# Optimization experiments

Hardware: AMD Instinct MI355X
Metric: run time of the kernel (lower is better)

## Reference

```python
import jax, jax.numpy as jnp
import numpy as np

SIZE = 256
R = 896          # total radial bins = nodes per sample (128 + 4*64 + 16*32)
LMAX = 510       # widest folded ring row (i=127 -> 4i+2)
WMAX = LMAX - 1  # conv output width (kernel=2)
HID = 32         # ConvAutoEncoder hidden channels (create_layers default)
ENC = 10         # hidden_encoder (per-bin embedding dim)
GCN_H = 64
NCLS = 10
B = 8
EPS = 7168       # edges per sample (avg degree 8)
PAD = 3 * SIZE * SIZE  # padding gather index -> zero column


def _reshape_2d(arr, border):
    # verbatim port of reshape_2d, applied to index arrays
    ptr_st, ptr_end = border, len(arr) - border
    d1 = list(arr[:ptr_st]); d2 = list(arr[ptr_end:])
    itt = 4
    while ptr_st != ptr_end:
        (d1 if itt > 2 else d2).append(arr[ptr_st])
        ptr_st += 1; itt -= 1
        if itt == 0:
            itt = 4
    return np.stack([d1, d2])


def build_static():
    # For each radial bin rad in 0..895: flat gather indices (into the
    # concatenated 3*256*256 per-sample maps) in boolean-mask (row-major)
    # order, folded by reshape_2d to (2, 4i+2), padded to LMAX with PAD.
    idx = np.full((R, 2, LMAX), PAD, np.int32)
    band = np.zeros(R, np.int32)
    rad = 0
    for m, coef in enumerate([1, 2, 4]):
        step = SIZE // coef
        c = step / 2 - 0.5
        ii, jj = np.meshgrid(np.arange(step), np.arange(step), indexing='ij')
        d = (np.maximum(np.abs(ii - c), np.abs(jj - c)) // 1).astype(int)  # create_circular
        for by in range(coef):
            for bx in range(coef):
                flat = m * SIZE * SIZE + (by * step + ii) * SIZE + (bx * step + jj)
                for i in range(step // 2):
                    sel = flat[d == i]                    # row-major ring pixels (8i+4)
                    two = _reshape_2d(sel, 2 + 2 * i)     # (2, 4i+2)
                    L = two.shape[1]
                    idx[rad, :, :L] = two
                    band[rad] = L - 1                     # band_length = 4i+1
                    rad += 1
    return idx, band


def gcn_conv(x, W, b, src, dst, ew, n):
    # torch_geometric GCNConv: add self loops (w=1), symmetric norm, aggregate at dst
    loop = jnp.arange(n)
    s = jnp.concatenate([src, loop])
    t = jnp.concatenate([dst, loop])
    w = jnp.concatenate([ew, jnp.ones((n,), x.dtype)])
    deg = jax.ops.segment_sum(w, t, num_segments=n)
    dinv = jnp.where(deg > 0, jax.lax.rsqrt(jnp.maximum(deg, 1e-12)), 0.0)
    norm = dinv[s] * w * dinv[t]
    xw = x @ W
    return jax.ops.segment_sum(norm[:, None] * xw[s], t, num_segments=n) + b


def setup_inputs() -> dict:
    key = jax.random.key(0)
    ks = jax.random.split(key, 12)
    idx_np, band = build_static()
    x = jax.random.normal(ks[0], (B, 3, SIZE, SIZE), jnp.float32)
    base = jax.random.randint(ks[1], (2, B, EPS), 0, R)
    edge_index = (base + (jnp.arange(B) * R)[None, :, None]).reshape(2, -1)
    batch_vec = jnp.arange(B * R, dtype=jnp.int32) // R
    Wconv = jax.random.normal(ks[2], (R, HID, 2, 2), jnp.float32) * 0.3
    bconv = jax.random.normal(ks[3], (R, HID), jnp.float32) * 0.05
    # decoder padded to WMAX, zeroed beyond each bin's band length (exact math)
    mask = (np.arange(WMAX)[None, :] < band[:, None]).astype(np.float32)
    Wdec = jax.random.normal(ks[4], (R, ENC, HID, WMAX), jnp.float32) * 0.02
    Wdec = Wdec * jnp.asarray(mask)[:, None, None, :]
    bdec = jax.random.normal(ks[5], (R, ENC), jnp.float32) * 0.05
    edge_w = jax.random.normal(ks[6], (EPS,), jnp.float32)
    Wg1 = jax.random.normal(ks[7], (ENC, GCN_H), jnp.float32) * (1.0 / np.sqrt(ENC))
    bg1 = jnp.zeros((GCN_H,), jnp.float32)
    Wg2 = jax.random.normal(ks[8], (GCN_H, GCN_H), jnp.float32) * (1.0 / np.sqrt(GCN_H))
    bg2 = jnp.zeros((GCN_H,), jnp.float32)
    Wl = jax.random.normal(ks[9], (GCN_H, NCLS), jnp.float32) * (1.0 / np.sqrt(GCN_H))
    bl = jnp.zeros((NCLS,), jnp.float32)
    return dict(x=x, edge_index=edge_index, batch_vec=batch_vec, idx=jnp.asarray(idx_np),
                Wconv=Wconv, bconv=bconv, Wdec=Wdec, bdec=bdec, edge_w=edge_w,
                Wg1=Wg1, bg1=bg1, Wg2=Wg2, bg2=bg2, Wl=Wl, bl=bl)


def reference(x, edge_index, batch_vec, idx, Wconv, bconv, Wdec, bdec, edge_w,
              Wg1, bg1, Wg2, bg2, Wl, bl):
    b = x.shape[0]
    n = b * R
    # --- get_embedding: batched radial-bin gather + per-bin 2x2 conv + linear ---
    xp = jnp.concatenate([x.reshape(b, -1), jnp.zeros((b, 1), x.dtype)], axis=1)
    vals = xp[:, idx]                                         # (B,R,2,LMAX)
    win = jnp.stack([vals[..., :-1], vals[..., 1:]], axis=-1)  # (B,R,2,WMAX,2) = b r kh w kw
    h = jax.nn.relu(jnp.einsum('brhwk,rchk->brcw', win, Wconv) + bconv[:, :, None])
    emb = jnp.einsum('brcw,rocw->bro', h, Wdec) + bdec         # (B,R,ENC)
    nodes = emb.reshape(n, ENC)
    # --- GCN: trainable sigmoid edge weights tiled per sample ---
    ew = jax.nn.sigmoid(jnp.tile(edge_w, b))
    src, dst = edge_index[0], edge_index[1]
    h1 = jax.nn.relu(gcn_conv(nodes, Wg1, bg1, src, dst, ew, n))
    h2 = gcn_conv(h1, Wg2, bg2, src, dst, ew, n)
    pooled = jax.ops.segment_sum(h2, batch_vec, num_segments=b) / R  # global_mean_pool (equal sizes)
    # dropout p=0.1 in eval mode -> identity
    return jax.nn.softmax(pooled @ Wl + bl, axis=1)
```

## Files before the change

kernel.cpp:

```cpp
#include <hip/hip_runtime.h>

static constexpr int kR    = 896;
static constexpr int kLMAX = 510;
static constexpr int kWMAX = 509;
static constexpr int kHID  = 32;
static constexpr int kENC  = 10;
static constexpr int kGH   = 64;
static constexpr int kNCLS = 10;
static constexpr int kB    = 8;
static constexpr int kEPS  = 7168;
static constexpr int kN    = kB * kR;
static constexpr int kE    = kB * kEPS;
static constexpr int kPAD  = 3 * 256 * 256;

constexpr int band_of(int r) {
    int i = (r < 128) ? r : (r < 384) ? ((r - 128) & 63) : ((r - 384) & 31);
    return 4 * i + 1;
}
__device__ __forceinline__ int band_dev(int r) {
    int i = (r < 128) ? r : (r < 384) ? ((r - 128) & 63) : ((r - 384) & 31);
    return 4 * i + 1;
}

static constexpr int kCHUNK = 128;
constexpr int count_chunks() {
    int n = 0;
    for (int r = 0; r < kR; ++r) n += (band_of(r) + kCHUNK - 1) / kCHUNK;
    return n;
}
static constexpr int kNCHUNK = count_chunks();
static_assert(kNCHUNK == 1216, "chunk count");

struct CE { short r; short w0; };
struct Tab { CE e[kNCHUNK]; };
constexpr Tab make_tab() {
    Tab t{};
    int n = 0;
    for (int r = 0; r < kR; ++r)
        for (int w0 = 0; w0 < band_of(r); w0 += kCHUNK) {
            t.e[n].r = (short)r; t.e[n].w0 = (short)w0; ++n;
        }
    return t;
}
__device__ __constant__ Tab g_tab = make_tab();

static constexpr size_t OFF_EMB  = 0;
static constexpr size_t OFF_DEG  = OFF_EMB + 71680;
static constexpr size_t OFF_CNT  = OFF_DEG + 7168;
static constexpr size_t OFF_POOL = OFF_CNT + 7168;
static constexpr size_t kMEMSET_FLOATS = OFF_POOL + 512;
static constexpr size_t OFF_DINV = kMEMSET_FLOATS;
static constexpr size_t OFF_CSUM = OFF_DINV + 7168;
static constexpr size_t OFF_OFFS = OFF_CSUM + 7168;
static constexpr size_t OFF_WOFF = OFF_OFFS + 7169;
static constexpr size_t OFF_CSRC = OFF_WOFF + 7169;
static constexpr size_t OFF_CNRM = OFF_CSRC + 57344;
static constexpr size_t OFF_XW1  = OFF_CNRM + 57344;
static constexpr size_t OFF_XT   = (OFF_XW1 + 458752 + 7) & ~(size_t)7;

__device__ __forceinline__ float sigmoidf_(float v) { return 1.0f / (1.0f + expf(-v)); }

__global__ __launch_bounds__(256)
void k_xpose(const float* __restrict__ x, const int* __restrict__ ei,
             const float* __restrict__ edge_w,
             float* __restrict__ xt, float* __restrict__ deg, int* __restrict__ cnt)
{
    const int bid = blockIdx.x;
    const int tid = threadIdx.x;
    if (bid < kPAD / 256) {
        const int j = bid * 256 + tid;
        float4 lo, hi;
        lo.x = x[(size_t)0 * kPAD + j]; lo.y = x[(size_t)1 * kPAD + j];
        lo.z = x[(size_t)2 * kPAD + j]; lo.w = x[(size_t)3 * kPAD + j];
        hi.x = x[(size_t)4 * kPAD + j]; hi.y = x[(size_t)5 * kPAD + j];
        hi.z = x[(size_t)6 * kPAD + j]; hi.w = x[(size_t)7 * kPAD + j];
        float4* dst = (float4*)&xt[(size_t)j * 8];
        dst[0] = lo; dst[1] = hi;
    } else {
        const int e = (bid - kPAD / 256) * 256 + tid;
        if (e < kE) {
            const int t = ei[kE + e];
            atomicAdd(&deg[t], sigmoidf_(edge_w[e % kEPS]));
            atomicAdd(&cnt[t], 1);
        }
    }
}

__global__ __launch_bounds__(320, 4)
void k_conv_emb(const float* __restrict__ xt, const int* __restrict__ idx,
                const float* __restrict__ Wconv, const float* __restrict__ bconv,
                const float* __restrict__ Wdec, float* __restrict__ emb)
{
    const int bid = blockIdx.x;
    const int tid = threadIdx.x;

    const int r     = g_tab.e[bid].r;
    const int w0    = g_tab.e[bid].w0;
    const int bandr = band_dev(r);
    const int wc    = min(kCHUNK, bandr - w0);

    __shared__ float vals[2][kB][kCHUNK + 1];
    __shared__ float wconv_s[kHID * 4];
    __shared__ float bconv_s[kHID];

    if (tid < 128) wconv_s[tid] = Wconv[r * 128 + tid];
    else if (tid < 160) bconv_s[tid - 128] = bconv[r * kHID + (tid - 128)];

    if (tid < 2 * (kCHUNK + 1)) {
        const int hh = tid >= (kCHUNK + 1);
        const int li = tid - hh * (kCHUNK + 1);
        const int j = (li <= wc) ? idx[(r * 2 + hh) * kLMAX + w0 + li] : kPAD;
        float4 lo = {0, 0, 0, 0}, hi = {0, 0, 0, 0};
        if ((unsigned)j < (unsigned)kPAD) {
            const float4* src = (const float4*)&xt[(size_t)j * 8];
            lo = src[0]; hi = src[1];
        }
        vals[hh][0][li] = lo.x; vals[hh][1][li] = lo.y;
        vals[hh][2][li] = lo.z; vals[hh][3][li] = lo.w;
        vals[hh][4][li] = hi.x; vals[hh][5][li] = hi.y;
        vals[hh][6][li] = hi.z; vals[hh][7][li] = hi.w;
    }
    __syncthreads();

    const int wave = tid >> 6, lane = tid & 63;
    const int o0 = wave * 2;
    const float* Wd0 = Wdec + ((size_t)(r * kENC + o0) * kHID) * kWMAX;
    const float* Wd1 = Wd0 + (size_t)kHID * kWMAX;

    float acc0[8] = {0,0,0,0,0,0,0,0}, acc1[8] = {0,0,0,0,0,0,0,0};

    #pragma unroll
    for (int st = 0; st < 2; ++st) {
        const int wl = st * 64 + lane;
        if (st * 64 >= wc) break;
        const bool valid = (wl < wc);
        const int w = w0 + wl;

        float v00[8], v01[8], v10[8], v11[8];
        #pragma unroll
        for (int b = 0; b < 8; ++b) {
            v00[b] = vals[0][b][wl]; v01[b] = vals[0][b][wl + 1];
            v10[b] = vals[1][b][wl]; v11[b] = vals[1][b][wl + 1];
        }

        #pragma unroll 8
        for (int c = 0; c < kHID; ++c) {
            const float wd0 = valid ? Wd0[(size_t)c * kWMAX + w] : 0.0f;
            const float wd1 = valid ? Wd1[(size_t)c * kWMAX + w] : 0.0f;
            const float w00 = wconv_s[c * 4 + 0], w01 = wconv_s[c * 4 + 1];
            const float w10 = wconv_s[c * 4 + 2], w11 = wconv_s[c * 4 + 3];
            const float bc  = bconv_s[c];
            #pragma unroll
            for (int b = 0; b < 8; ++b) {
                float h = fmaf(v00[b], w00, fmaf(v01[b], w01,
                          fmaf(v10[b], w10, fmaf(v11[b], w11, bc))));
                h = fmaxf(h, 0.0f);
                acc0[b] = fmaf(wd0, h, acc0[b]);
                acc1[b] = fmaf(wd1, h, acc1[b]);
            }
        }
    }

    #pragma unroll
    for (int b = 0; b < 8; ++b) {
        float s0 = acc0[b], s1 = acc1[b];
        #pragma unroll
        for (int sft = 32; sft > 0; sft >>= 1) {
            s0 += __shfl_xor(s0, sft);
            s1 += __shfl_xor(s1, sft);
        }
        if (lane == 0) {
            atomicAdd(&emb[((size_t)b * kR + r) * kENC + o0],     s0);
            atomicAdd(&emb[((size_t)b * kR + r) * kENC + o0 + 1], s1);
        }
    }
}

__global__ __launch_bounds__(256)
void k_scanxw1(const float* __restrict__ deg, const int* __restrict__ cnt,
               float* __restrict__ dinv, float* __restrict__ colsum,
               int* __restrict__ off, int* __restrict__ woff,
               const float* __restrict__ emb, const float* __restrict__ bdec,
               const float* __restrict__ Wg1, float* __restrict__ xw1)
{
    const int bid = blockIdx.x;
    const int t = threadIdx.x;
    if (bid > 0) {
        const int tt = (bid - 1) * 256 + t;
        const int i = tt >> 6, f = tt & 63;
        const int r = i % kR;
        float s = 0.0f;
        #pragma unroll
        for (int o = 0; o < kENC; ++o)
            s = fmaf(emb[i * kENC + o] + bdec[r * kENC + o], Wg1[o * kGH + f], s);
        xw1[tt] = s;
        return;
    }

    for (int i = t; i < kN; i += 256) {
        float d = deg[i] + 1.0f;
        dinv[i]   = rsqrtf(d);
        colsum[i] = 1.0f / d;
    }
    __shared__ int cl[kN];
    for (int i = t; i < kN; i += 256) cl[i] = cnt[i];
    __syncthreads();

    int loc[28];
    int s = 0;
    const int base = t * 28;
    #pragma unroll
    for (int k = 0; k < 28; ++k) { loc[k] = s; s += cl[base + k]; }

    __shared__ int sa[256], sb[256];
    sa[t] = s;
    __syncthreads();
    int* in = sa; int* out = sb;
    for (int d = 1; d < 256; d <<= 1) {
        out[t] = in[t] + ((t >= d) ? in[t - d] : 0);
        __syncthreads();
        int* tmp = in; in = out; out = tmp;
    }
    const int incl = in[t];
    const int excl = incl - s;
    #pragma unroll
    for (int k = 0; k < 28; ++k) {
        off[base + k]  = excl + loc[k];
        woff[base + k] = excl + loc[k];
    }
    if (t == 255) off[kN] = incl;
}

__global__ __launch_bounds__(256)
void k_fill(const int* __restrict__ ei, const float* __restrict__ edge_w,
            const float* __restrict__ dinv, int* __restrict__ woff,
            int* __restrict__ csrc, float* __restrict__ cnrm,
            float* __restrict__ colsum)
{
    int e = blockIdx.x * 256 + threadIdx.x;
    if (e >= kE) return;
    const int s = ei[e], t = ei[kE + e];
    const float nm = dinv[s] * sigmoidf_(edge_w[e % kEPS]) * dinv[t];
    const int p = atomicAdd(&woff[t], 1);
    csrc[p] = s;
    cnrm[p] = nm;
    atomicAdd(&colsum[s], nm);
}

__global__ __launch_bounds__(256)
void k_agg(const float* __restrict__ xw1, const int* __restrict__ off,
           const int* __restrict__ csrc, const float* __restrict__ cnrm,
           const float* __restrict__ dinv, const float* __restrict__ colsum,
           const float* __restrict__ bg1, const float* __restrict__ Wg2,
           float* __restrict__ pooled)
{
    const int tid  = threadIdx.x;
    const int wave = tid >> 6, f = tid & 63;

    __shared__ float wg2s[kGH * kGH];
    __shared__ float hrow[4][kGH];
    __shared__ float pool_s[kGH];

    for (int i = tid; i < kGH * kGH; i += 256) wg2s[i] = Wg2[i];
    if (tid < kGH) pool_s[tid] = 0.0f;
    __syncthreads();

    const int j0 = blockIdx.x * 16;
    #pragma unroll
    for (int q = 0; q < 4; ++q) {
        const int j = j0 + wave * 4 + q;
        const float di = dinv[j];
        float a = fmaf(di * di, xw1[(size_t)j * kGH + f], bg1[f]);
        const int pb = off[j], pe = off[j + 1];
        int   sC = 0; float nC = 0.0f;
        if (pb < pe) { sC = csrc[pb]; nC = cnrm[pb]; }
        for (int p = pb; p < pe; ++p) {
            int sN = sC; float nN = 0.0f;
            if (p + 1 < pe) { sN = csrc[p + 1]; nN = cnrm[p + 1]; }
            a = fmaf(nC, xw1[(size_t)sC * kGH + f], a);
            sC = sN; nC = nN;
        }
        a = fmaxf(a, 0.0f);
        hrow[wave][f] = a;
        float s2 = 0.0f;
        #pragma unroll 8
        for (int f2 = 0; f2 < kGH; ++f2)
            s2 = fmaf(hrow[wave][f2], wg2s[f2 * kGH + f], s2);
        atomicAdd(&pool_s[f], colsum[j] * s2);
    }
    __syncthreads();
    if (tid < kGH) {
        const int b = j0 / kR;
        atomicAdd(&pooled[b * kGH + tid], pool_s[tid]);
    }
}

__global__ __launch_bounds__(128)
void k_head(const float* __restrict__ pooled, const float* __restrict__ bg2,
            const float* __restrict__ Wl, const float* __restrict__ bl,
            float* __restrict__ out)
{
    const int t = threadIdx.x;
    __shared__ float lgs[kB * kNCLS];
    if (t < kB * kNCLS) {
        const int b = t / kNCLS, c = t % kNCLS;
        float s = bl[c];
        for (int g = 0; g < kGH; ++g) {
            const float pg = bg2[g] + pooled[b * kGH + g] * (1.0f / kR);
            s = fmaf(pg, Wl[g * kNCLS + c], s);
        }
        lgs[t] = s;
    }
    __syncthreads();
    if (t < kB) {
        float mx = lgs[t * kNCLS];
        for (int j = 1; j < kNCLS; ++j) mx = fmaxf(mx, lgs[t * kNCLS + j]);
        float ssum = 0.0f, ex[kNCLS];
        for (int j = 0; j < kNCLS; ++j) { ex[j] = expf(lgs[t * kNCLS + j] - mx); ssum += ex[j]; }
        for (int j = 0; j < kNCLS; ++j) out[t * kNCLS + j] = ex[j] / ssum;
    }
}

extern "C" void kernel_launch(void* const* d_in, const int* in_sizes, int n_in,
                              void* d_out, int out_size, void* d_ws, size_t ws_size,
                              hipStream_t stream)
{
    const float* x      = (const float*)d_in[0];
    const int*   ei     = (const int*)d_in[1];
    const int*   idx    = (const int*)d_in[3];
    const float* Wconv  = (const float*)d_in[4];
    const float* bconv  = (const float*)d_in[5];
    const float* Wdec   = (const float*)d_in[6];
    const float* bdec   = (const float*)d_in[7];
    const float* edge_w = (const float*)d_in[8];
    const float* Wg1    = (const float*)d_in[9];
    const float* bg1    = (const float*)d_in[10];
    const float* Wg2    = (const float*)d_in[11];
    const float* bg2    = (const float*)d_in[12];
    const float* Wl     = (const float*)d_in[13];
    const float* bl     = (const float*)d_in[14];

    float* ws     = (float*)d_ws;
    float* emb    = ws + OFF_EMB;
    float* deg    = ws + OFF_DEG;
    int*   cnt    = (int*)(ws + OFF_CNT);
    float* pooled = ws + OFF_POOL;
    float* dinv   = ws + OFF_DINV;
    float* colsum = ws + OFF_CSUM;
    int*   off    = (int*)(ws + OFF_OFFS);
    int*   woff   = (int*)(ws + OFF_WOFF);
    int*   csrc   = (int*)(ws + OFF_CSRC);
    float* cnrm   = ws + OFF_CNRM;
    float* xw1    = ws + OFF_XW1;
    float* xt     = ws + OFF_XT;

    hipMemsetAsync(ws, 0, kMEMSET_FLOATS * sizeof(float), stream);

    k_xpose<<<kPAD / 256 + (kE + 255) / 256, 256, 0, stream>>>(x, ei, edge_w, xt, deg, cnt);

    k_conv_emb<<<kNCHUNK, 320, 0, stream>>>(xt, idx, Wconv, bconv, Wdec, emb);

    k_scanxw1<<<1 + kN * kGH / 256, 256, 0, stream>>>(deg, cnt, dinv, colsum, off, woff,
                                                      emb, bdec, Wg1, xw1);
    k_fill<<<(kE + 255) / 256, 256, 0, stream>>>(ei, edge_w, dinv, woff, csrc, cnrm, colsum);
    k_agg <<<kN / 16, 256, 0, stream>>>(xw1, off, csrc, cnrm, dinv, colsum, bg1, Wg2, pooled);
    k_head<<<1, 128, 0, stream>>>(pooled, bg2, Wl, bl, (float*)d_out);
}
```

Baseline: 122.3 us.

## Compute five output channels per wave in conv-embedding kernel with 128-thread blocks

Shrinks the conv_emb block from five waves to two, with each wave now accumulating five output channels instead of two. The ReLU conv activation h is computed once and reused across five decoder weights, which cuts the redundant conv FMA work by a factor of 2.5. The block's gather load loop is rewritten to stride over 128 threads. In exchange each thread holds more accumulator registers (40 instead of 16), and each block has fewer waves to hide memory latency.

```diff
diff --git a/kernel.cpp b/kernel.cpp
--- a/kernel.cpp
+++ b/kernel.cpp
@@ -86,7 +86,7 @@
     }
 }
 
-__global__ __launch_bounds__(320, 4)
+__global__ __launch_bounds__(128, 3)
 void k_conv_emb(const float* __restrict__ xt, const int* __restrict__ idx,
                 const float* __restrict__ Wconv, const float* __restrict__ bconv,
                 const float* __restrict__ Wdec, float* __restrict__ emb)
@@ -103,12 +103,12 @@
     __shared__ float wconv_s[kHID * 4];
     __shared__ float bconv_s[kHID];
 
-    if (tid < 128) wconv_s[tid] = Wconv[r * 128 + tid];
-    else if (tid < 160) bconv_s[tid - 128] = bconv[r * kHID + (tid - 128)];
-
-    if (tid < 2 * (kCHUNK + 1)) {
-        const int hh = tid >= (kCHUNK + 1);
-        const int li = tid - hh * (kCHUNK + 1);
+    wconv_s[tid] = Wconv[r * 128 + tid];
+    if (tid < kHID) bconv_s[tid] = bconv[r * kHID + tid];
+
+    for (int i = tid; i < 2 * (kCHUNK + 1); i += 128) {
+        const int hh = i >= (kCHUNK + 1);
+        const int li = i - hh * (kCHUNK + 1);
         const int j = (li <= wc) ? idx[(r * 2 + hh) * kLMAX + w0 + li] : kPAD;
         float4 lo = {0, 0, 0, 0}, hi = {0, 0, 0, 0};
         if ((unsigned)j < (unsigned)kPAD) {
@@ -123,16 +123,19 @@
     __syncthreads();
 
     const int wave = tid >> 6, lane = tid & 63;
-    const int o0 = wave * 2;
-    const float* Wd0 = Wdec + ((size_t)(r * kENC + o0) * kHID) * kWMAX;
-    const float* Wd1 = Wd0 + (size_t)kHID * kWMAX;
-
-    float acc0[8] = {0,0,0,0,0,0,0,0}, acc1[8] = {0,0,0,0,0,0,0,0};
+    const int og = wave * 5;
+    const float* Wbase = Wdec + (size_t)(r * kENC + og) * kHID * kWMAX;
+
+    float acc0[8] = {0,0,0,0,0,0,0,0};
+    float acc1[8] = {0,0,0,0,0,0,0,0};
+    float acc2[8] = {0,0,0,0,0,0,0,0};
+    float acc3[8] = {0,0,0,0,0,0,0,0};
+    float acc4[8] = {0,0,0,0,0,0,0,0};
 
     #pragma unroll
     for (int st = 0; st < 2; ++st) {
+        if (st * 64 >= wc) break;
         const int wl = st * 64 + lane;
-        if (st * 64 >= wc) break;
         const bool valid = (wl < wc);
         const int w = w0 + wl;
 
@@ -143,10 +146,19 @@
             v10[b] = vals[1][b][wl]; v11[b] = vals[1][b][wl + 1];
         }
 
+        const float* W0 = Wbase + (size_t)0 * kHID * kWMAX + w;
+        const float* W1 = Wbase + (size_t)1 * kHID * kWMAX + w;
+        const float* W2 = Wbase + (size_t)2 * kHID * kWMAX + w;
+        const float* W3 = Wbase + (size_t)3 * kHID * kWMAX + w;
+        const float* W4 = Wbase + (size_t)4 * kHID * kWMAX + w;
+
         #pragma unroll 8
         for (int c = 0; c < kHID; ++c) {
-            const float wd0 = valid ? Wd0[(size_t)c * kWMAX + w] : 0.0f;
-            const float wd1 = valid ? Wd1[(size_t)c * kWMAX + w] : 0.0f;
+            const float wd0 = valid ? W0[(size_t)c * kWMAX] : 0.0f;
+            const float wd1 = valid ? W1[(size_t)c * kWMAX] : 0.0f;
+            const float wd2 = valid ? W2[(size_t)c * kWMAX] : 0.0f;
+            const float wd3 = valid ? W3[(size_t)c * kWMAX] : 0.0f;
+            const float wd4 = valid ? W4[(size_t)c * kWMAX] : 0.0f;
             const float w00 = wconv_s[c * 4 + 0], w01 = wconv_s[c * 4 + 1];
             const float w10 = wconv_s[c * 4 + 2], w11 = wconv_s[c * 4 + 3];
             const float bc  = bconv_s[c];
@@ -157,21 +169,31 @@
                 h = fmaxf(h, 0.0f);
                 acc0[b] = fmaf(wd0, h, acc0[b]);
                 acc1[b] = fmaf(wd1, h, acc1[b]);
+                acc2[b] = fmaf(wd2, h, acc2[b]);
+                acc3[b] = fmaf(wd3, h, acc3[b]);
+                acc4[b] = fmaf(wd4, h, acc4[b]);
             }
         }
     }
 
     #pragma unroll
     for (int b = 0; b < 8; ++b) {
-        float s0 = acc0[b], s1 = acc1[b];
+        float s0 = acc0[b], s1 = acc1[b], s2 = acc2[b], s3 = acc3[b], s4 = acc4[b];
         #pragma unroll
         for (int sft = 32; sft > 0; sft >>= 1) {
             s0 += __shfl_xor(s0, sft);
             s1 += __shfl_xor(s1, sft);
+            s2 += __shfl_xor(s2, sft);
+            s3 += __shfl_xor(s3, sft);
+            s4 += __shfl_xor(s4, sft);
         }
         if (lane == 0) {
-            atomicAdd(&emb[((size_t)b * kR + r) * kENC + o0],     s0);
-            atomicAdd(&emb[((size_t)b * kR + r) * kENC + o0 + 1], s1);
+            float* ep = &emb[((size_t)b * kR + r) * kENC + og];
+            atomicAdd(ep + 0, s0);
+            atomicAdd(ep + 1, s1);
+            atomicAdd(ep + 2, s2);
+            atomicAdd(ep + 3, s3);
+            atomicAdd(ep + 4, s4);
         }
     }
 }
@@ -358,7 +380,7 @@
 
     k_xpose<<<kPAD / 256 + (kE + 255) / 256, 256, 0, stream>>>(x, ei, edge_w, xt, deg, cnt);
 
-    k_conv_emb<<<kNCHUNK, 320, 0, stream>>>(xt, idx, Wconv, bconv, Wdec, emb);
+    k_conv_emb<<<kNCHUNK, 128, 0, stream>>>(xt, idx, Wconv, bconv, Wdec, emb);
 
     k_scanxw1<<<1 + kN * kGH / 256, 256, 0, stream>>>(deg, cnt, dinv, colsum, off, woff,
                                                       emb, bdec, Wg1, xw1);
```

Measured after the change: 150.0 us. 1.23x slower.
